# Kernel tuning notes

Measured on AMD Instinct MI355X. Metric: run time of the kernel, lower is better.

Reference implementation:

```python
import jax, jax.numpy as jnp
import numpy as np

N_CLASSES = 19


def setup_inputs() -> dict:
    key = jax.random.key(0)
    k1, k2 = jax.random.split(key)
    embedding = jax.random.normal(k1, (4, 32, 128, 128), dtype=jnp.float32)
    label = jax.random.randint(k2, (4, 512, 512), 0, N_CLASSES, dtype=jnp.int64)
    return {"embedding": embedding, "label": label}


def _discriminative_loss(embedding, label, n_classes=N_CLASSES):
    N, H, W = label.shape
    C = embedding.shape[1]
    # bilinear upsample embedding to label resolution (F.upsample mode='bilinear')
    emb = jax.image.resize(embedding, (N, C, H, W), method="bilinear")
    HW = H * W
    emb = emb.reshape(N, C, HW).transpose(0, 2, 1)          # (N, HW, C)
    lab = label.reshape(N, HW)                               # (N, HW)

    onehot = jax.nn.one_hot(lab, n_classes, dtype=emb.dtype)  # (N, HW, K)
    count = onehot.sum(1)                                    # (N, K)
    mask = (count > 0).astype(emb.dtype)                     # (N, K)

    # per-class embedding sum and (biased, /(count+1)) mean
    cls_sum = jnp.einsum("npc,npk->nkc", emb, onehot)       # (N, K, C)
    cls_mean = cls_sum / (count[:, :, None] + 1.0)           # (N, K, C)

    # intra-class: per-pixel squared distance to own-class mean, mean over C
    mean_pp = jnp.take_along_axis(cls_mean, lab[:, :, None], axis=1)  # (N, HW, C)
    d2 = jnp.mean((emb - mean_pp) ** 2, axis=-1)             # (N, HW)
    intra_per_cls = jnp.einsum("np,npk->nk", d2, onehot) / (count + 1.0)  # (N, K)
    n_fg = mask[:, 1:].sum(1)                                # (N,)
    l2_intra = (intra_per_cls[:, 1:] * mask[:, 1:]).sum(1) / n_fg  # (N,)

    # inter-class: pairwise mean squared distance between class means
    diff = cls_mean[:, :, None, :] - cls_mean[:, None, :, :]  # (N, K, K, C)
    inter = jnp.mean(diff ** 2, axis=-1)                     # (N, K, K)
    inter = inter * mask[:, None, :] * mask[:, :, None]
    l2_inter = inter[:, 1:, 1:].reshape(N, -1).sum(1) / (n_fg * n_fg)  # (N,)

    return l2_intra - l2_inter


def reference(embedding, label):
    return _discriminative_loss(embedding, label)
```

## Files before the change

### kernel.cpp

```cpp
#include <hip/hip_runtime.h>

#define NIMG 4
#define NCLS 19
#define CCH  32
#define LH   128
#define LW   128
#define HH   512
#define WW   512
#define HWQ  (LH*LW)
#define HWP  (HH*WW)

#define TR 8
#define TC 8
#define NTX (LW/TC)
#define NTILE (256)
#define TCELLS (TR*TC)
#define RW 10
#define RING 100
#define NSLOT 608

__device__ __forceinline__ void taps(int v, int lim, int& i0, float& w0, float& w1) {
    int r = v & 3;
    int b = (v >> 2) + ((r < 2) ? -1 : 0);
    float f = 0.125f + 0.25f * (float)((r + 2) & 3);
    w0 = 1.f - f; w1 = f;
    if (b < 0)           { b = 0;       w0 = 1.f; w1 = 0.f; }
    else if (b >= lim)   { b = lim - 1; w0 = 0.f; w1 = 1.f; }
    i0 = b;
}

__device__ __forceinline__ float ring_fetch(const float* Gn, int i, int Y0, int X0) {
    int p = i / RING, r = i - p * RING;
    int gy = r / RW, gx = r - gy * RW;
    int yy = Y0 - 1 + gy; yy = yy < 0 ? 0 : (yy > LH - 1 ? LH - 1 : yy);
    int xx = X0 - 1 + gx; xx = xx < 0 ? 0 : (xx > LW - 1 ? LW - 1 : xx);
    return Gn[(size_t)p * HWQ + yy * LW + xx];
}

__global__ __launch_bounds__(256) void k_gram(const float* __restrict__ E,
        float* __restrict__ G, float* __restrict__ AccCS) {
    int n = blockIdx.y, rp = blockIdx.x;
    int tid = threadIdx.x;
    if (n == 0 && rp == 0 && tid < NIMG * 2 * NCLS) AccCS[tid] = 0.f;
    int x = tid & 127, dy = tid >> 7;
    int y = rp * 2 + dy;
    int yn = (y < LH - 1) ? y + 1 : y;
    int xn = (x < LW - 1) ? x + 1 : x;
    bool fix = ((x & 63) == 63);
    const float* base = E + (size_t)n * CCH * HWQ;
    const float* Ea = base + y * LW + x;
    const float* Eb = base + yn * LW + x;
    const float* Eax = base + y * LW + xn;
    const float* Ebx = base + yn * LW + xn;
    float gs = 0.f, gh = 0.f, gv = 0.f, gda = 0.f;
#pragma unroll 8
    for (int c = 0; c < CCH; c++) {
        float a = Ea[(size_t)c * HWQ];
        float b = Eb[(size_t)c * HWQ];
        float ar = __shfl_down(a, 1);
        float br = __shfl_down(b, 1);
        if (fix) { ar = Eax[(size_t)c * HWQ]; br = Ebx[(size_t)c * HWQ]; }
        gs = fmaf(a, a, gs);
        gh = fmaf(a, ar, gh);
        gv = fmaf(a, b, gv);
        gda = fmaf(a, br, fmaf(ar, b, gda));
    }
    float* Gp = G + (size_t)n * 4 * HWQ + y * LW + x;
    Gp[0] = gs; Gp[HWQ] = gh; Gp[2 * HWQ] = gv; Gp[3 * HWQ] = gda;
}

__global__ __launch_bounds__(256, 4) void k_field(const float* __restrict__ E,
        const int* __restrict__ lab, const float* __restrict__ G,
        float* __restrict__ P_sumT, float* __restrict__ AccCS) {
    int tile = blockIdx.x, n = blockIdx.y;
    int ty = tile >> 4, tx = tile & 15;
    int Y0 = ty * TR, X0 = tx * TC;
    __shared__ float A[TCELLS * NCLS];
    __shared__ float Gt[4 * RING];
    __shared__ float S2w[4 * NCLS];
    __shared__ float tmpc[NCLS * 8];
    int tid = threadIdx.x;
    const int* ln = lab + (size_t)n * HWP;
    int h_lo = Y0 * 4 - 2;

    int hA, qA, hB = 0, qB = 0; bool vB;
    int4 LA, LB = make_int4(0, 0, 0, 0);
    {
        int hr = tid / RW, qi = tid - hr * RW;
        hA = h_lo + hr; qA = X0 - 1 + qi;
        int hc = hA < 0 ? 0 : (hA > HH - 1 ? HH - 1 : hA);
        int qc = qA < 0 ? 0 : (qA > LW - 1 ? LW - 1 : qA);
        LA = *(const int4*)(ln + hc * WW + (qc << 2));
    }
    vB = (tid < 360 - 256);
    if (vB) {
        int i = tid + 256;
        int hr = i / RW, qi = i - hr * RW;
        hB = h_lo + hr; qB = X0 - 1 + qi;
        int hc = hB < 0 ? 0 : (hB > HH - 1 ? HH - 1 : hB);
        int qc = qB < 0 ? 0 : (qB > LW - 1 ? LW - 1 : qB);
        LB = *(const int4*)(ln + hc * WW + (qc << 2));
    }
    int cc = tid >> 3, cy = tid & 7;
    const float* Er = E + ((size_t)n * CCH + cc) * HWQ + (Y0 + cy) * LW + X0;
    float4 ev0 = *(const float4*)Er;
    float4 ev1 = *(const float4*)(Er + 4);
    const float* Gn = G + (size_t)n * 4 * HWQ;
    float rv0 = ring_fetch(Gn, tid, Y0, X0);
    bool rB = (tid < 4 * RING - 256);
    float rv1 = rB ? ring_fetch(Gn, tid + 256, Y0, X0) : 0.f;

    for (int i = tid; i < TCELLS * NCLS; i += 256) A[i] = 0.f;
    if (tid < 4 * NCLS) S2w[tid] = 0.f;
    Gt[tid] = rv0;
    if (rB) Gt[tid + 256] = rv1;
    __syncthreads();

    const float* Gs_ = Gt, *Gh_ = Gt + RING, *Gv_ = Gt + 2 * RING, *Gda_ = Gt + 3 * RING;
    auto process = [&](int h, int q, int4 l4) {
        if (h < 0 || h >= HH || q < 0 || q >= LW) return;
        int y0; float wy0, wy1;
        taps(h, LH - 1, y0, wy0, wy1);
        int ry = y0 - Y0;
        bool r0 = (unsigned)ry < (unsigned)TR, r1 = (unsigned)(ry + 1) < (unsigned)TR;
        int rxm = q - 1 - X0, rx0 = q - X0, rxp = q + 1 - X0;
        bool bm = (unsigned)rxm < (unsigned)TC, b0 = (unsigned)rx0 < (unsigned)TC,
             bp = (unsigned)rxp < (unsigned)TC;
        bool fast = (q >= 1) && (q <= 126);
        bool owned = ((unsigned)(h - Y0 * 4) < 32u) && b0;
        if (fast) {
            if (r0) {
                int rb = (ry * TC) * NCLS;
                if (bm) { float* a = &A[rb + rxm * NCLS];
                    atomicAdd(a + l4.x, wy0 * 0.375f); atomicAdd(a + l4.y, wy0 * 0.125f); }
                if (b0) { float* a = &A[rb + rx0 * NCLS];
                    atomicAdd(a + l4.x, wy0 * 0.625f); atomicAdd(a + l4.y, wy0 * 0.875f);
                    atomicAdd(a + l4.z, wy0 * 0.875f); atomicAdd(a + l4.w, wy0 * 0.625f); }
                if (bp) { float* a = &A[rb + rxp * NCLS];
                    atomicAdd(a + l4.z, wy0 * 0.125f); atomicAdd(a + l4.w, wy0 * 0.375f); }
            }
            if (r1) {
                int rb = ((ry + 1) * TC) * NCLS;
                if (bm) { float* a = &A[rb + rxm * NCLS];
                    atomicAdd(a + l4.x, wy1 * 0.375f); atomicAdd(a + l4.y, wy1 * 0.125f); }
                if (b0) { float* a = &A[rb + rx0 * NCLS];
                    atomicAdd(a + l4.x, wy1 * 0.625f); atomicAdd(a + l4.y, wy1 * 0.875f);
                    atomicAdd(a + l4.z, wy1 * 0.875f); atomicAdd(a + l4.w, wy1 * 0.625f); }
                if (bp) { float* a = &A[rb + rxp * NCLS];
                    atomicAdd(a + l4.z, wy1 * 0.125f); atomicAdd(a + l4.w, wy1 * 0.375f); }
            }
            if (owned) {
                float u0 = wy0 * wy0, u1 = wy1 * wy1, u2t = 2.f * wy0 * wy1;
                int g00 = (y0 - Y0 + 1) * RW + rx0;
                float C0 = u0 * Gs_[g00]     + u1 * Gs_[g00 + RW]     + u2t * Gv_[g00];
                float C1 = u0 * Gs_[g00 + 1] + u1 * Gs_[g00 + RW + 1] + u2t * Gv_[g00 + 1];
                float C2 = u0 * Gs_[g00 + 2] + u1 * Gs_[g00 + RW + 2] + u2t * Gv_[g00 + 2];
                float D0 = 2.f * (u0 * Gh_[g00]     + u1 * Gh_[g00 + RW])     + u2t * Gda_[g00];
                float D1 = 2.f * (u0 * Gh_[g00 + 1] + u1 * Gh_[g00 + RW + 1]) + u2t * Gda_[g00 + 1];
                float d2a = fmaf(0.140625f, C0, fmaf(0.390625f, C1, 0.46875f * D0));
                float d2b = fmaf(0.015625f, C0, fmaf(0.765625f, C1, 0.21875f * D0));
                float d2c = fmaf(0.765625f, C1, fmaf(0.015625f, C2, 0.21875f * D1));
                float d2d = fmaf(0.390625f, C1, fmaf(0.140625f, C2, 0.46875f * D1));
                int wv = (tid >> 6) * NCLS;
                atomicAdd(&S2w[wv + l4.x], d2a); atomicAdd(&S2w[wv + l4.y], d2b);
                atomicAdd(&S2w[wv + l4.z], d2c); atomicAdd(&S2w[wv + l4.w], d2d);
            }
        } else {
            int Ls[4] = {l4.x, l4.y, l4.z, l4.w};
            float u0 = wy0 * wy0, u1 = wy1 * wy1, u2t = 2.f * wy0 * wy1;
            int gyr = y0 - Y0 + 1;
            int wv = (tid >> 6) * NCLS;
#pragma unroll
            for (int j = 0; j < 4; j++) {
                int w = (q << 2) + j;
                int x0; float wx0, wx1;
                taps(w, LW - 1, x0, wx0, wx1);
                int rxa = x0 - X0, rxb = rxa + 1;
                int L = Ls[j];
                if (r0) {
                    int rb = (ry * TC) * NCLS;
                    if ((unsigned)rxa < (unsigned)TC) atomicAdd(&A[rb + rxa * NCLS + L], wy0 * wx0);
                    if ((unsigned)rxb < (unsigned)TC) atomicAdd(&A[rb + rxb * NCLS + L], wy0 * wx1);
                }
                if (r1) {
                    int rb = ((ry + 1) * TC) * NCLS;
                    if ((unsigned)rxa < (unsigned)TC) atomicAdd(&A[rb + rxa * NCLS + L], wy1 * wx0);
                    if ((unsigned)rxb < (unsigned)TC) atomicAdd(&A[rb + rxb * NCLS + L], wy1 * wx1);
                }
                if (owned) {
                    int gg = gyr * RW + (x0 - X0 + 1);
                    float Ca = u0 * Gs_[gg]     + u1 * Gs_[gg + RW]     + u2t * Gv_[gg];
                    float Cb = u0 * Gs_[gg + 1] + u1 * Gs_[gg + RW + 1] + u2t * Gv_[gg + 1];
                    float Dd = 2.f * (u0 * Gh_[gg] + u1 * Gh_[gg + RW]) + u2t * Gda_[gg];
                    float d2 = wx0 * wx0 * Ca + wx1 * wx1 * Cb + 2.f * wx0 * wx1 * Dd;
                    atomicAdd(&S2w[wv + L], d2);
                }
            }
        }
    };
    process(hA, qA, LA);
    if (vB) process(hB, qB, LB);
    __syncthreads();

    {
        float ev[8] = {ev0.x, ev0.y, ev0.z, ev0.w, ev1.x, ev1.y, ev1.z, ev1.w};
        float acc[NCLS];
#pragma unroll
        for (int k = 0; k < NCLS; k++) acc[k] = 0.f;
#pragma unroll
        for (int cx = 0; cx < 8; cx++) {
            const float* Ar = &A[(cy * 8 + cx) * NCLS];
            float e = ev[cx];
#pragma unroll
            for (int k = 0; k < NCLS; k++) acc[k] = fmaf(Ar[k], e, acc[k]);
        }
#pragma unroll
        for (int k = 0; k < NCLS; k++) {
            acc[k] += __shfl_xor(acc[k], 1);
            acc[k] += __shfl_xor(acc[k], 2);
            acc[k] += __shfl_xor(acc[k], 4);
        }
        if (cy == 0) {
            float* pt = P_sumT + ((size_t)n * NSLOT + cc) * NTILE + tile;
#pragma unroll
            for (int k = 0; k < NCLS; k++) pt[(size_t)k * 32 * NTILE] = acc[k];
        }
    }
    if (tid < 8 * NCLS) {
        int g8 = tid / NCLS, k = tid - g8 * NCLS;
        float s = 0.f;
#pragma unroll
        for (int j = 0; j < 8; j++) s += A[(g8 * 8 + j) * NCLS + k];
        tmpc[k * 8 + g8] = s;
    }
    __syncthreads();
    if (tid < NCLS) {
        float s = 0.f;
#pragma unroll
        for (int g8 = 0; g8 < 8; g8++) s += tmpc[tid * 8 + g8];
        atomicAdd(&AccCS[n * 2 * NCLS + tid], s);
        float s2 = S2w[tid] + S2w[NCLS + tid] + S2w[2 * NCLS + tid] + S2w[3 * NCLS + tid];
        atomicAdd(&AccCS[n * 2 * NCLS + NCLS + tid], s2);
    }
}

__global__ __launch_bounds__(256) void k_final(const float* __restrict__ P_sumT,
        const float* __restrict__ AccCS, float* __restrict__ out) {
    int n = blockIdx.x, tid = threadIdx.x;
    __shared__ double cs_d[NCLS * 33];
    __shared__ double m_d[NCLS * 33];
    __shared__ double cnt_d[NCLS], s2_d[NCLS];
    __shared__ double wpart[4];
    __shared__ double sIntra, sNfg;

    for (int idx = tid; idx < NSLOT; idx += 256) {
        const float4* p4 = (const float4*)(P_sumT + ((size_t)n * NSLOT + idx) * NTILE);
        double s = 0.0;
#pragma unroll 4
        for (int j = 0; j < NTILE / 4; j++) {
            float4 v = p4[j];
            s += (double)((v.x + v.y) + (v.z + v.w));
        }
        cs_d[(idx >> 5) * 33 + (idx & 31)] = s;
    }
    if (tid < NCLS) {
        cnt_d[tid] = (double)AccCS[n * 2 * NCLS + tid];
        s2_d[tid]  = (double)AccCS[n * 2 * NCLS + NCLS + tid];
    }
    __syncthreads();
    for (int idx = tid; idx < NSLOT; idx += 256) {
        int k = idx >> 5, c = idx & 31;
        m_d[k * 33 + c] = cs_d[k * 33 + c] / (cnt_d[k] + 1.0);
    }
    __syncthreads();
    double vi = 0.0, fg = 0.0;
    if (tid >= 1 && tid < NCLS && cnt_d[tid] > 0.0) {
        fg = 1.0;
        double dot = 0.0, mm = 0.0;
        for (int c = 0; c < CCH; c++) {
            double mv = m_d[tid * 33 + c];
            dot += mv * cs_d[tid * 33 + c];
            mm += mv * mv;
        }
        vi = (s2_d[tid] - 2.0 * dot + cnt_d[tid] * mm) * 0.03125 / (cnt_d[tid] + 1.0);
    }
    if (tid < 64) {
#pragma unroll
        for (int s_ = 32; s_ >= 1; s_ >>= 1) { vi += __shfl_xor(vi, s_); fg += __shfl_xor(fg, s_); }
        if (tid == 0) { sIntra = vi; sNfg = fg; }
    }
    double ve = 0.0;
    for (int t2 = tid; t2 < 324; t2 += 256) {
        int j = 1 + t2 / 18, k = 1 + t2 % 18;
        if (cnt_d[j] > 0.0 && cnt_d[k] > 0.0) {
            double s = 0.0;
            for (int c = 0; c < CCH; c++) {
                double d = m_d[j * 33 + c] - m_d[k * 33 + c];
                s += d * d;
            }
            ve += s * 0.03125;
        }
    }
#pragma unroll
    for (int s_ = 32; s_ >= 1; s_ >>= 1) ve += __shfl_xor(ve, s_);
    if ((tid & 63) == 0) wpart[tid >> 6] = ve;
    __syncthreads();
    if (tid == 0) {
        double inter = wpart[0] + wpart[1] + wpart[2] + wpart[3];
        out[n] = (float)(sIntra / sNfg - inter / (sNfg * sNfg));
    }
}

extern "C" void kernel_launch(void* const* d_in, const int* in_sizes, int n_in,
                              void* d_out, int out_size, void* d_ws, size_t ws_size,
                              hipStream_t stream) {
    const float* E = (const float*)d_in[0];
    const int* lab = (const int*)d_in[1];
    float* out = (float*)d_out;

    float* P_sumT = (float*)d_ws;
    float* AccCS  = P_sumT + (size_t)NIMG * NSLOT * NTILE;
    float* G      = AccCS + NIMG * 2 * NCLS;

    k_gram <<<dim3(64, NIMG),    dim3(256), 0, stream>>>(E, G, AccCS);
    k_field<<<dim3(NTILE, NIMG), dim3(256), 0, stream>>>(E, lab, G, P_sumT, AccCS);
    k_final<<<dim3(NIMG),        dim3(256), 0, stream>>>(P_sumT, AccCS, out);
}
```

Before: 143.1 us.

## Stage per-tile class sums in LDS and replace atomics with per-tile partials

```diff
diff --git a/kernel.cpp b/kernel.cpp
--- a/kernel.cpp
+++ b/kernel.cpp
@@ -38,10 +38,9 @@
 }
 
 __global__ __launch_bounds__(256) void k_gram(const float* __restrict__ E,
-        float* __restrict__ G, float* __restrict__ AccCS) {
+        float* __restrict__ G) {
     int n = blockIdx.y, rp = blockIdx.x;
     int tid = threadIdx.x;
-    if (n == 0 && rp == 0 && tid < NIMG * 2 * NCLS) AccCS[tid] = 0.f;
     int x = tid & 127, dy = tid >> 7;
     int y = rp * 2 + dy;
     int yn = (y < LH - 1) ? y + 1 : y;
@@ -71,7 +70,7 @@
 
 __global__ __launch_bounds__(256, 4) void k_field(const float* __restrict__ E,
         const int* __restrict__ lab, const float* __restrict__ G,
-        float* __restrict__ P_sumT, float* __restrict__ AccCS) {
+        float* __restrict__ P_sum, float* __restrict__ P_cnt, float* __restrict__ P_S2) {
     int tile = blockIdx.x, n = blockIdx.y;
     int ty = tile >> 4, tx = tile & 15;
     int Y0 = ty * TR, X0 = tx * TC;
@@ -79,6 +78,7 @@
     __shared__ float Gt[4 * RING];
     __shared__ float S2w[4 * NCLS];
     __shared__ float tmpc[NCLS * 8];
+    __shared__ __align__(16) float cs_l[NSLOT];
     int tid = threadIdx.x;
     const int* ln = lab + (size_t)n * HWP;
     int h_lo = Y0 * 4 - 2;
@@ -221,9 +221,8 @@
             acc[k] += __shfl_xor(acc[k], 4);
         }
         if (cy == 0) {
-            float* pt = P_sumT + ((size_t)n * NSLOT + cc) * NTILE + tile;
-#pragma unroll
-            for (int k = 0; k < NCLS; k++) pt[(size_t)k * 32 * NTILE] = acc[k];
+#pragma unroll
+            for (int k = 0; k < NCLS; k++) cs_l[k * CCH + cc] = acc[k];
         }
     }
     if (tid < 8 * NCLS) {
@@ -234,38 +233,58 @@
         tmpc[k * 8 + g8] = s;
     }
     __syncthreads();
+
+    float* Ps = P_sum + (size_t)(n * NTILE + tile) * NSLOT;
+    if (tid < NSLOT / 4) ((float4*)Ps)[tid] = ((const float4*)cs_l)[tid];
     if (tid < NCLS) {
         float s = 0.f;
 #pragma unroll
         for (int g8 = 0; g8 < 8; g8++) s += tmpc[tid * 8 + g8];
-        atomicAdd(&AccCS[n * 2 * NCLS + tid], s);
-        float s2 = S2w[tid] + S2w[NCLS + tid] + S2w[2 * NCLS + tid] + S2w[3 * NCLS + tid];
-        atomicAdd(&AccCS[n * 2 * NCLS + NCLS + tid], s2);
-    }
-}
-
-__global__ __launch_bounds__(256) void k_final(const float* __restrict__ P_sumT,
-        const float* __restrict__ AccCS, float* __restrict__ out) {
+        P_cnt[(size_t)(n * NTILE + tile) * NCLS + tid] = s;
+        P_S2[(size_t)(n * NTILE + tile) * NCLS + tid] =
+            S2w[tid] + S2w[NCLS + tid] + S2w[2 * NCLS + tid] + S2w[3 * NCLS + tid];
+    }
+}
+
+__global__ __launch_bounds__(256) void k_final(const float* __restrict__ P_sum,
+        const float* __restrict__ P_cnt, const float* __restrict__ P_S2,
+        float* __restrict__ out) {
     int n = blockIdx.x, tid = threadIdx.x;
     __shared__ double cs_d[NCLS * 33];
     __shared__ double m_d[NCLS * 33];
     __shared__ double cnt_d[NCLS], s2_d[NCLS];
+    __shared__ double rk1[NCLS * 9], rk2[NCLS * 9];
     __shared__ double wpart[4];
     __shared__ double sIntra, sNfg;
 
-    for (int idx = tid; idx < NSLOT; idx += 256) {
-        const float4* p4 = (const float4*)(P_sumT + ((size_t)n * NSLOT + idx) * NTILE);
-        double s = 0.0;
+    for (int i4 = tid; i4 < NSLOT / 4; i4 += 256) {
+        const float4* p4 = (const float4*)(P_sum + (size_t)n * NTILE * NSLOT) + i4;
+        double sx = 0.0, sy = 0.0, sz = 0.0, sw = 0.0;
 #pragma unroll 4
-        for (int j = 0; j < NTILE / 4; j++) {
-            float4 v = p4[j];
-            s += (double)((v.x + v.y) + (v.z + v.w));
-        }
-        cs_d[(idx >> 5) * 33 + (idx & 31)] = s;
-    }
+        for (int t = 0; t < NTILE; t++) {
+            float4 v = p4[(size_t)t * (NSLOT / 4)];
+            sx += v.x; sy += v.y; sz += v.z; sw += v.w;
+        }
+        int idx = i4 * 4;
+        int k = idx >> 5, c = idx & 31;
+        cs_d[k * 33 + c] = sx; cs_d[k * 33 + c + 1] = sy;
+        cs_d[k * 33 + c + 2] = sz; cs_d[k * 33 + c + 3] = sw;
+    }
+    if (tid < 8 * NCLS) {
+        int k = tid >> 3, g = tid & 7;
+        const float* p1 = P_cnt + ((size_t)n * NTILE + g * 32) * NCLS + k;
+        const float* p2 = P_S2  + ((size_t)n * NTILE + g * 32) * NCLS + k;
+        double s1 = 0.0, s2 = 0.0;
+#pragma unroll 4
+        for (int j = 0; j < 32; j++) { s1 += p1[j * NCLS]; s2 += p2[j * NCLS]; }
+        rk1[k * 9 + g] = s1; rk2[k * 9 + g] = s2;
+    }
+    __syncthreads();
     if (tid < NCLS) {
-        cnt_d[tid] = (double)AccCS[n * 2 * NCLS + tid];
-        s2_d[tid]  = (double)AccCS[n * 2 * NCLS + NCLS + tid];
+        double s1 = 0.0, s2 = 0.0;
+#pragma unroll
+        for (int g = 0; g < 8; g++) { s1 += rk1[tid * 9 + g]; s2 += rk2[tid * 9 + g]; }
+        cnt_d[tid] = s1; s2_d[tid] = s2;
     }
     __syncthreads();
     for (int idx = tid; idx < NSLOT; idx += 256) {
@@ -318,11 +337,12 @@
     const int* lab = (const int*)d_in[1];
     float* out = (float*)d_out;
 
-    float* P_sumT = (float*)d_ws;
-    float* AccCS  = P_sumT + (size_t)NIMG * NSLOT * NTILE;
-    float* G      = AccCS + NIMG * 2 * NCLS;
-
-    k_gram <<<dim3(64, NIMG),    dim3(256), 0, stream>>>(E, G, AccCS);
-    k_field<<<dim3(NTILE, NIMG), dim3(256), 0, stream>>>(E, lab, G, P_sumT, AccCS);
-    k_final<<<dim3(NIMG),        dim3(256), 0, stream>>>(P_sumT, AccCS, out);
-}
+    float* P_sum = (float*)d_ws;
+    float* P_cnt = P_sum + (size_t)NIMG * NTILE * NSLOT;
+    float* P_S2  = P_cnt + (size_t)NIMG * NTILE * NCLS;
+    float* G     = P_S2  + (size_t)NIMG * NTILE * NCLS;
+
+    k_gram <<<dim3(64, NIMG),    dim3(256), 0, stream>>>(E, G);
+    k_field<<<dim3(NTILE, NIMG), dim3(256), 0, stream>>>(E, lab, G, P_sum, P_cnt, P_S2);
+    k_final<<<dim3(NIMG),        dim3(256), 0, stream>>>(P_sum, P_cnt, P_S2, out);
+}
```

Measured after the change: 141.4 us. About the same (-1.2%).
